# Kernel tuning notes

Measured on AMD Instinct MI355X. Metric: run time of the kernel, lower is better.

## Reference

```python
import jax, jax.numpy as jnp
import numpy as np

B, S, HID = 1, 2048, 2048
H, KVH, D, VD = 32, 8, 128, 128
R = 64  # rope_dim = head_dim * partial_rotary_factor, rounded down to even
N_REP = H // KVH
SCALE = D ** -0.5
NEG = -1e9


def _rotate_half(x):
    half = x.shape[-1] // 2
    return jnp.concatenate([-x[..., half:], x[..., :half]], axis=-1)


def setup_inputs() -> dict:
    key = jax.random.key(0)
    ks = jax.random.split(key, 8)
    hidden_states = jax.random.normal(ks[0], (B, S, HID), dtype=jnp.float32)
    # RoPE angles: standard inverse-frequency positional embedding of width R
    inv_freq = 1.0 / (10000.0 ** (np.arange(0, R, 2, dtype=np.float32) / R))
    pos = np.arange(S, dtype=np.float32)
    freqs = np.outer(pos, inv_freq)                       # [S, R/2]
    emb = np.concatenate([freqs, freqs], axis=-1)         # [S, R]
    cos = jnp.asarray(np.cos(emb))[None].repeat(B, axis=0)  # [B, S, R]
    sin = jnp.asarray(np.sin(emb))[None].repeat(B, axis=0)
    # additive causal mask [B, 1, S, S]
    causal = jnp.triu(jnp.full((S, S), NEG, dtype=jnp.float32), k=1)
    attention_mask = jnp.broadcast_to(causal[None, None], (B, 1, S, S))
    std = 0.02
    Wq = jax.random.normal(ks[1], (H * D, HID), dtype=jnp.float32) * std
    Wk = jax.random.normal(ks[2], (KVH * D, HID), dtype=jnp.float32) * std
    Wv = jax.random.normal(ks[3], (KVH * VD, HID), dtype=jnp.float32) * std
    Wo = jax.random.normal(ks[4], (HID, H * VD), dtype=jnp.float32) * std
    sink_bias = jax.random.normal(ks[5], (H,), dtype=jnp.float32) * 0.5
    return {"hidden_states": hidden_states, "cos": cos, "sin": sin,
            "attention_mask": attention_mask, "Wq": Wq, "Wk": Wk, "Wv": Wv,
            "Wo": Wo, "sink_bias": sink_bias}


def reference(hidden_states, cos, sin, attention_mask, Wq, Wk, Wv, Wo, sink_bias):
    b, s, _ = hidden_states.shape
    # projections -> [B, heads, S, dim]
    q = (hidden_states @ Wq.T).reshape(b, s, H, D).transpose(0, 2, 1, 3)
    k = (hidden_states @ Wk.T).reshape(b, s, KVH, D).transpose(0, 2, 1, 3)
    v = (hidden_states @ Wv.T).reshape(b, s, KVH, VD).transpose(0, 2, 1, 3)
    # partial RoPE on first R dims
    c = cos[:, None, :, :]  # [B,1,S,R]
    si = sin[:, None, :, :]
    q_r, q_n = q[..., :R], q[..., R:]
    k_r, k_n = k[..., :R], k[..., R:]
    q = jnp.concatenate([q_r * c + _rotate_half(q_r) * si, q_n], axis=-1)
    k = jnp.concatenate([k_r * c + _rotate_half(k_r) * si, k_n], axis=-1)
    # GQA: repeat kv heads
    k_rep = jnp.repeat(k, N_REP, axis=1)
    v_rep = jnp.repeat(v, N_REP, axis=1)
    scores = jnp.einsum('bhqd,bhkd->bhqk', q, k_rep) * SCALE + attention_mask
    # extra attention-sink logit column per head
    sinks = jnp.broadcast_to(sink_bias.reshape(1, H, 1, 1), (b, H, s, 1))
    aw = jnp.concatenate([scores, sinks], axis=-1)            # [B,H,S,S+1]
    probs = jax.nn.softmax(aw, axis=-1)[..., :-1]             # drop sink column
    out = jnp.einsum('bhqk,bhkd->bhqd', probs, v_rep)
    out = out.transpose(0, 2, 1, 3).reshape(b, s, H * VD)
    return out @ Wo.T
```

## Files before the change

kernel.cpp:

```cpp
#include <hip/hip_runtime.h>

typedef unsigned short u16;
typedef unsigned int   u32;
typedef __bf16  bf16x8 __attribute__((ext_vector_type(8)));
typedef float   f32x4  __attribute__((ext_vector_type(4)));
typedef float   f32x16 __attribute__((ext_vector_type(16)));
typedef u16     u16x4  __attribute__((ext_vector_type(4)));
typedef u16     u16x8  __attribute__((ext_vector_type(8)));
typedef u32     u32x4  __attribute__((ext_vector_type(4)));

#define S_LEN 2048
#define NH 32
#define NKVH 8
#define HD 128
#define QKVST 6144
#define AOST  4096
#define ATT_SCALE 0.08838834764831845f
#define LOG2E 1.4426950408889634f
#define QSC2 (ATT_SCALE * LOG2E)
#define RESCALE_THR2 11.5f
#define PARTSZ 16640

__device__ __forceinline__ u16 f2bf(float f){
  u32 u = __builtin_bit_cast(u32, f);
  u += 0x7FFFu + ((u >> 16) & 1u);
  return (u16)(u >> 16);
}
__device__ __forceinline__ float bf2f(u16 h){
  u32 u = ((u32)h) << 16;
  return __builtin_bit_cast(float, u);
}
__device__ __forceinline__ u32 cvtpk(float lo, float hi){
  u32 d;
  asm("v_cvt_pk_bf16_f32 %0, %1, %2" : "=v"(d) : "v"(lo), "v"(hi));
  return d;
}
__device__ __forceinline__ void gload_lds16(const u16* g, u16* l){
  __builtin_amdgcn_global_load_lds(
      (const __attribute__((address_space(1))) void*)g,
      (__attribute__((address_space(3))) void*)l, 16, 0, 0);
}

__global__ void cvt_all_kernel(const f32x4* __restrict__ hs, const f32x4* __restrict__ wq,
                               const f32x4* __restrict__ wk, const f32x4* __restrict__ wv,
                               const f32x4* __restrict__ wo, u16x4* __restrict__ out){
  int i = blockIdx.x * 256 + threadIdx.x;
  const f32x4* src; int off;
  if      (i < 1048576){ src = hs; off = i; }
  else if (i < 3145728){ src = wq; off = i - 1048576; }
  else if (i < 3670016){ src = wk; off = i - 3145728; }
  else if (i < 4194304){ src = wv; off = i - 3670016; }
  else                 { src = wo; off = i - 4194304; }
  f32x4 v = src[off];
  u16x4 o;
  o[0] = f2bf(v[0]); o[1] = f2bf(v[1]); o[2] = f2bf(v[2]); o[3] = f2bf(v[3]);
  out[i] = o;
}

template<int OUT_BF16, int ROPE, int BM, int BN, int BK>
__global__ __launch_bounds__(256, 2)
void gemm_bt_kernel(const u16* __restrict__ X, const u16* __restrict__ W,
                    void* __restrict__ Cv, int M, int N, int K,
                    const float* __restrict__ cosv, const float* __restrict__ sinv){
  const int NS = BK / 32;
  __shared__ __align__(16) u16 As[2][NS][BM * 32];
  __shared__ __align__(16) u16 Bs[2][NS][BN * 32];
  const int MI = BM / 32, NJ = BN / 32;
  const int m0 = blockIdx.y * BM, n0 = blockIdx.x * BN;
  const int tid = threadIdx.x;
  const int wave = tid >> 6, lane = tid & 63;
  const int wm = wave >> 1, wn = wave & 1;
  const int g = lane >> 4, ln = lane & 15;
  const int r0 = tid >> 2;
  const int cc = (((tid & 3) ^ ((r0 >> 1) & 3)) * 8);
  f32x4 acc[MI][NJ] = {};
  const u16* xa0 = X + (size_t)(m0 + r0) * K + cc;
  const u16* xa1 = X + (size_t)(m0 + r0 + 64) * K + (((tid & 3) ^ (((r0 + 64) >> 1) & 3)) * 8);
  const u16* wb0 = W + (size_t)(n0 + r0) * K + cc;
  const u16* wb1 = W + (size_t)(n0 + r0 + 64) * K + (((tid & 3) ^ (((r0 + 64) >> 1) & 3)) * 8);

  auto stage = [&](int buf, int k0){
    #pragma unroll
    for (int s = 0; s < NS; s++){
      const int kc = k0 + s * 32;
      gload_lds16(xa0 + kc, &As[buf][s][tid * 8]);
      if (BM == 128) gload_lds16(xa1 + kc, &As[buf][s][2048 + tid * 8]);
      gload_lds16(wb0 + kc, &Bs[buf][s][tid * 8]);
      if (BN == 128) gload_lds16(wb1 + kc, &Bs[buf][s][2048 + tid * 8]);
    }
  };

  stage(0, 0);
  __syncthreads();
  int cur = 0;
  for (int k0 = 0; k0 < K; k0 += BK){
    if (k0 + BK < K) stage(cur ^ 1, k0 + BK);
    #pragma unroll
    for (int s = 0; s < NS; s++){
      bf16x8 a[MI], b[NJ];
      #pragma unroll
      for (int f = 0; f < MI; f++){
        const int row = wm * (BM / 2) + f * 16 + ln;
        a[f] = *(const bf16x8*)&As[cur][s][row * 32 + ((g ^ ((row >> 1) & 3)) * 8)];
      }
      #pragma unroll
      for (int f = 0; f < NJ; f++){
        const int row = wn * (BN / 2) + f * 16 + ln;
        b[f] = *(const bf16x8*)&Bs[cur][s][row * 32 + ((g ^ ((row >> 1) & 3)) * 8)];
      }
      __builtin_amdgcn_s_setprio(1);
      #pragma unroll
      for (int i = 0; i < MI; i++)
        #pragma unroll
        for (int j = 0; j < NJ; j++)
          acc[i][j] = __builtin_amdgcn_mfma_f32_16x16x32_bf16(a[i], b[j], acc[i][j], 0, 0, 0);
      __builtin_amdgcn_s_setprio(0);
    }
    __syncthreads();
    cur ^= 1;
  }
  if (ROPE && BN == 128){
    if (wn == 0 && n0 < 5120){
      #pragma unroll
      for (int i = 0; i < MI; i++)
        #pragma unroll
        for (int r = 0; r < 4; r++){
          const int row = m0 + wm * (BM / 2) + i * 16 + g * 4 + r;
          #pragma unroll
          for (int j = 0; j < 2; j++){
            const int d = j * 16 + ln;
            float c  = cosv[row * 64 + d];
            float sn = sinv[row * 64 + d];
            float x0 = acc[i][j][r], x1 = acc[i][j + 2][r];
            acc[i][j][r]     = x0 * c - x1 * sn;
            acc[i][j + 2][r] = x1 * c + x0 * sn;
          }
        }
    }
    if (n0 < 4096){
      #pragma unroll
      for (int i = 0; i < MI; i++)
        #pragma unroll
        for (int j = 0; j < NJ; j++)
          #pragma unroll
          for (int r = 0; r < 4; r++) acc[i][j][r] *= QSC2;
    }
  }
  #pragma unroll
  for (int i = 0; i < MI; i++)
    #pragma unroll
    for (int j = 0; j < NJ; j++)
      #pragma unroll
      for (int r = 0; r < 4; r++){
        int row = m0 + wm * (BM / 2) + i * 16 + g * 4 + r;
        int col = n0 + wn * (BN / 2) + j * 16 + ln;
        if (OUT_BF16) ((u16*)Cv)[(size_t)row * N + col] = f2bf(acc[i][j][r]);
        else          ((float*)Cv)[(size_t)row * N + col] = acc[i][j][r];
      }
}

__global__ void vtrans_kernel(const u16* __restrict__ QKV, u16* __restrict__ VT){
  int idx = blockIdx.x * 256 + threadIdx.x;
  if (idx >= NKVH * HD * S_LEN) return;
  int s   = idx & (S_LEN - 1);
  int vd  = (idx >> 11) & (HD - 1);
  int kvh = idx >> 18;
  VT[idx] = QKV[(size_t)s * QKVST + 5120 + kvh * HD + vd];
}

__global__ __launch_bounds__(256, 2)
void attn_kernel(const u16* __restrict__ QKV, const u16* __restrict__ VT,
                 const float* __restrict__ sinkb, u16* __restrict__ AO,
                 u16* __restrict__ PART){
  __shared__ __align__(16) u16 Ks[2][32 * 256];
  __shared__ __align__(16) u16 Vs[2][32 * 256];
  const int b    = blockIdx.x;
  const int kvh  = b & 7;
  const int head = kvh * 4 + ((b >> 3) & 3);
  const int p    = (b >> 5) & 7;
  const int role = b >> 8;
  const int qtL  = 15 - p;
  const int tid  = threadIdx.x;
  const int w    = tid >> 6;
  const int lane = tid & 63;
  const int l31  = lane & 31, hi = lane >> 5;

  const u16* Kbase = QKV + 4096 + kvh * HD;
  const u16* Vbase = VT + (size_t)kvh * HD * S_LEN;

  auto stage = [&](int buf, int kt){
    const int k0 = kt * 64;
    #pragma unroll
    for (int pp = 0; pp < 4; pp++){
      int idx = pp * 256 + tid;
      int r = idx >> 5, c = idx & 31;
      int cs = c ^ r;
      int key = r * 2 + (cs >> 4), d8 = (cs & 15) * 8;
      gload_lds16(Kbase + (size_t)(k0 + key) * QKVST + d8, &Ks[buf][idx * 8]);
    }
    #pragma unroll
    for (int pp = 0; pp < 4; pp++){
      int idx = pp * 256 + tid;
      int r = idx >> 5, c = idx & 31;
      int cs = c ^ r;
      int vd = r * 4 + (cs >> 3), k8 = (cs & 7) * 8;
      gload_lds16(Vbase + (size_t)vd * S_LEN + k0 + k8, &Vs[buf][idx * 8]);
    }
  };

  const float sb2 = sinkb[head] * LOG2E;
  bf16x8 qB[8];
  float m, Ll;
  f32x16 O[4];

  auto load_q = [&](int q0){
    const int qw = q0 + w * 32;
    const u16* qrow = QKV + (size_t)(qw + l31) * QKVST + head * HD;
    #pragma unroll
    for (int t = 0; t < 8; t++) qB[t] = *(const bf16x8*)(qrow + t * 16 + hi * 8);
    #pragma unroll
    for (int n = 0; n < 4; n++) O[n] = f32x16{};
  };

  auto do_tile = [&](int cur, int k0, int qw){
    const u16* Kc = Ks[cur];
    const u16* Vc = Vs[cur];
    f32x16 sc0 = {}, sc1 = {};
    const int krow0 = (l31 >> 1);
    const int kc0   = ((l31 & 1) << 4) | hi;
    __builtin_amdgcn_s_setprio(1);
    #pragma unroll
    for (int t = 0; t < 8; t++){
      bf16x8 ka0 = *(const bf16x8*)&Kc[krow0 * 256 + ((kc0 + 2 * t) ^ krow0) * 8];
      bf16x8 ka1 = *(const bf16x8*)&Kc[(16 + krow0) * 256 + ((kc0 + 2 * t) ^ (16 + krow0)) * 8];
      sc0 = __builtin_amdgcn_mfma_f32_32x32x16_bf16(ka0, qB[t], sc0, 0, 0, 0);
      sc1 = __builtin_amdgcn_mfma_f32_32x32x16_bf16(ka1, qB[t], sc1, 0, 0, 0);
    }
    __builtin_amdgcn_s_setprio(0);

    if (k0 + 63 > qw){
      const int qg = qw + l31;
      #pragma unroll
      for (int r = 0; r < 16; r++){
        int keyr = k0 + (r & 3) + 8 * (r >> 2) + 4 * hi;
        if (keyr      > qg) sc0[r] = -1e30f;
        if (keyr + 32 > qg) sc1[r] = -1e30f;
      }
    }
    float mx = sc0[0];
    #pragma unroll
    for (int r = 1; r < 16; r++) mx = fmaxf(mx, sc0[r]);
    #pragma unroll
    for (int r = 0; r < 16; r++) mx = fmaxf(mx, sc1[r]);
    mx = fmaxf(mx, __shfl_xor(mx, 32));
    if (!__all(mx <= m + RESCALE_THR2)){
      float mn = fmaxf(m, mx);
      float sf = exp2f(m - mn);
      m = mn;
      #pragma unroll
      for (int n = 0; n < 4; n++)
        #pragma unroll
        for (int r = 0; r < 16; r++) O[n][r] *= sf;
      Ll *= sf;
    }
    float p0[16], p1[16];
    #pragma unroll
    for (int r = 0; r < 16; r++){ p0[r] = exp2f(sc0[r] - m); Ll += p0[r]; }
    #pragma unroll
    for (int r = 0; r < 16; r++){ p1[r] = exp2f(sc1[r] - m); Ll += p1[r]; }

    __builtin_amdgcn_s_setprio(1);
    #pragma unroll
    for (int c = 0; c < 4; c++){
      const float* ps = (c & 2) ? p1 : p0;
      const int bb = (c & 1) * 8;
      u32 wa = cvtpk(ps[bb + 0], ps[bb + 1]);
      u32 wb = cvtpk(ps[bb + 2], ps[bb + 3]);
      u32 wc = cvtpk(ps[bb + 4], ps[bb + 5]);
      u32 wd = cvtpk(ps[bb + 6], ps[bb + 7]);
      asm("v_permlane32_swap_b32 %0, %1" : "+v"(wa), "+v"(wc));
      asm("v_permlane32_swap_b32 %0, %1" : "+v"(wb), "+v"(wd));
      u32x4 wv_; wv_[0] = wa; wv_[1] = wb; wv_[2] = wc; wv_[3] = wd;
      bf16x8 pf = __builtin_bit_cast(bf16x8, wv_);
      #pragma unroll
      for (int n = 0; n < 4; n++){
        const int vrow = n * 8 + (l31 >> 2);
        const int vcc  = ((l31 & 3) << 3) | (c << 1) | hi;
        bf16x8 va = *(const bf16x8*)&Vc[vrow * 256 + (vcc ^ vrow) * 8];
        O[n] = __builtin_amdgcn_mfma_f32_32x32x16_bf16(va, pf, O[n], 0, 0, 0);
      }
    }
    __builtin_amdgcn_s_setprio(0);
  };

  auto run = [&](int q0, int kt0, int kt1){
    const int qw = q0 + w * 32;
    stage(0, kt0);
    __syncthreads();
    int cur = 0;
    for (int kt = kt0; kt < kt1; kt++){
      if (kt + 1 < kt1) stage(cur ^ 1, kt + 1);
      if (kt * 64 < qw + 32) do_tile(cur, kt * 64, qw);
      __syncthreads();
      cur ^= 1;
    }
  };

  auto epilogue = [&](int q0, bool final_, int rr_){
    float l = Ll + __shfl_xor(Ll, 32);
    float inv, lse;
    if (l > 0.f){ inv = 1.f / l; lse = m + __log2f(l); }
    else        { inv = 0.f;     lse = -1e30f; }
    u16* arena = &Ks[0][0];
    #pragma unroll
    for (int n = 0; n < 4; n++)
      #pragma unroll
      for (int r = 0; r < 16; r++){
        int vd = n * 32 + (r & 3) + 8 * (r >> 2) + 4 * hi;
        int ch = (vd >> 3) ^ (l31 & 15);
        arena[w * 4096 + l31 * 128 + ch * 8 + (vd & 7)] = f2bf(O[n][r] * inv);
      }
    __syncthreads();
    if (final_){
      #pragma unroll
      for (int pp = 0; pp < 8; pp++){
        int idx = pp * 256 + tid;
        int row = idx >> 4, c = idx & 15;
        u16x8 v = *(const u16x8*)&arena[row * 128 + ((c ^ (row & 15)) * 8)];
        *(u16x8*)&AO[(size_t)(q0 + row) * AOST + head * HD + c * 8] = v;
      }
    } else {
      u16* base = PART + (size_t)((head * 8 + p) * 2 + rr_) * PARTSZ;
      #pragma unroll
      for (int pp = 0; pp < 8; pp++){
        int idx = pp * 256 + tid;
        int row = idx >> 4, c = idx & 15;
        u16x8 v = *(const u16x8*)&arena[row * 128 + ((c ^ (row & 15)) * 8)];
        *(u16x8*)&base[row * 128 + c * 8] = v;
      }
      if (hi == 0) ((float*)(base + 16384))[w * 32 + l31] = lse;
    }
    __syncthreads();
  };

  const int q0L = qtL * 128;
  if (role == 0){
    load_q(q0L);
    m = sb2; Ll = (hi == 0) ? 1.f : 0.f;
    run(q0L, 0, 18);
    epilogue(q0L, false, 0);
  } else {
    load_q(q0L);
    m = -3.0e38f; Ll = 0.f;
    run(q0L, 18, 32 - 2 * p);
    epilogue(q0L, false, 1);
    const int q0S = p * 128;
    load_q(q0S);
    m = sb2; Ll = (hi == 0) ? 1.f : 0.f;
    run(q0S, 0, 2 * p + 2);
    epilogue(q0S, true, 0);
  }
}

__global__ void merge_kernel(const u16* __restrict__ PART, u16* __restrict__ AO){
  const int sidx = blockIdx.x;
  const int h = sidx >> 3, p = sidx & 7;
  const int q0 = (15 - p) * 128;
  const u16* A = PART + (size_t)(sidx * 2 + 0) * PARTSZ;
  const u16* B = PART + (size_t)(sidx * 2 + 1) * PARTSZ;
  const float* lseA = (const float*)(A + 16384);
  const float* lseB = (const float*)(B + 16384);
  #pragma unroll
  for (int it = 0; it < 8; it++){
    int idx = it * 256 + threadIdx.x;
    int row = idx >> 4, c = (idx & 15) * 8;
    float la = lseA[row], lb = lseB[row];
    float mx = fmaxf(la, lb);
    float wa = exp2f(la - mx), wb = exp2f(lb - mx);
    float inv = 1.f / (wa + wb);
    u16x8 va = *(const u16x8*)&A[row * 128 + c];
    u16x8 vb = *(const u16x8*)&B[row * 128 + c];
    u16x8 o;
    #pragma unroll
    for (int j = 0; j < 8; j++)
      o[j] = f2bf((bf2f(va[j]) * wa + bf2f(vb[j]) * wb) * inv);
    *(u16x8*)&AO[(size_t)(q0 + row) * AOST + h * HD + c] = o;
  }
}

extern "C" void kernel_launch(void* const* d_in, const int* in_sizes, int n_in,
                              void* d_out, int out_size, void* d_ws, size_t ws_size,
                              hipStream_t stream){
  (void)in_sizes; (void)n_in; (void)out_size; (void)ws_size;
  const float* hs    = (const float*)d_in[0];
  const float* cosv  = (const float*)d_in[1];
  const float* sinv  = (const float*)d_in[2];
  const float* Wq    = (const float*)d_in[4];
  const float* Wk    = (const float*)d_in[5];
  const float* Wv    = (const float*)d_in[6];
  const float* Wo    = (const float*)d_in[7];
  const float* sinkb = (const float*)d_in[8];
  float* out = (float*)d_out;

  char* ws = (char*)d_ws;
  u16* XB    = (u16*)(ws);
  u16* WQKVB = (u16*)(ws + 8388608);
  u16* WOB   = (u16*)(ws + 33554432);
  u16* QKV   = (u16*)(ws + 50331648);
  u16* VT    = (u16*)(ws + 75497472);
  u16* AO    = (u16*)(ws + 79691776);
  u16* PART  = (u16*)(ws);

  cvt_all_kernel<<<24576, 256, 0, stream>>>((const f32x4*)hs, (const f32x4*)Wq,
                                            (const f32x4*)Wk, (const f32x4*)Wv,
                                            (const f32x4*)Wo, (u16x4*)ws);

  gemm_bt_kernel<1, 1, 128, 128, 32><<<dim3(48, 16), 256, 0, stream>>>(XB, WQKVB, QKV, 2048, 6144, 2048, cosv, sinv);

  vtrans_kernel<<<8192, 256, 0, stream>>>(QKV, VT);

  attn_kernel<<<dim3(512), 256, 0, stream>>>(QKV, VT, sinkb, AO, PART);

  merge_kernel<<<dim3(256), 256, 0, stream>>>(PART, AO);

  gemm_bt_kernel<0, 0, 128, 64, 64><<<dim3(32, 16), 256, 0, stream>>>(AO, WOB, out, 2048, 2048, 4096, nullptr, nullptr);
}
```

Before: 220.0 us.

## Share K/V tiles across the four GQA heads in one 512-thread attention block

The attention kernel now runs 512-thread blocks in which 8 waves cover all four query heads of a KV group (2 waves per head, 64 query rows). Each K/V tile is staged into LDS once and used by all four heads, where before a separate block per head loaded it. The causal split into long/short query tiles and the partial-result merge are reworked for 64-row tiles, giving half as many blocks and larger partial buffers. The aim is to cut redundant K/V global loads, at the cost of fewer, larger blocks and possibly lower occupancy and load balance on the GPU.

```diff
diff --git a/kernel.cpp b/kernel.cpp
--- a/kernel.cpp
+++ b/kernel.cpp
@@ -19,7 +19,7 @@
 #define LOG2E 1.4426950408889634f
 #define QSC2 (ATT_SCALE * LOG2E)
 #define RESCALE_THR2 11.5f
-#define PARTSZ 16640
+#define PARTSZ 33280
 
 __device__ __forceinline__ u16 f2bf(float f){
   u32 u = __builtin_bit_cast(u32, f);
@@ -168,20 +168,19 @@
   VT[idx] = QKV[(size_t)s * QKVST + 5120 + kvh * HD + vd];
 }
 
-__global__ __launch_bounds__(256, 2)
+__global__ __launch_bounds__(512, 2)
 void attn_kernel(const u16* __restrict__ QKV, const u16* __restrict__ VT,
                  const float* __restrict__ sinkb, u16* __restrict__ AO,
                  u16* __restrict__ PART){
-  __shared__ __align__(16) u16 Ks[2][32 * 256];
-  __shared__ __align__(16) u16 Vs[2][32 * 256];
+  __shared__ __align__(16) u16 lds[4][32 * 256];
   const int b    = blockIdx.x;
   const int kvh  = b & 7;
-  const int head = kvh * 4 + ((b >> 3) & 3);
-  const int p    = (b >> 5) & 7;
-  const int role = b >> 8;
-  const int qtL  = 15 - p;
+  const int s    = (b >> 3) & 15;
+  const int role = b >> 7;
+  const int qtL  = 31 - s;
   const int tid  = threadIdx.x;
   const int w    = tid >> 6;
+  const int head = kvh * 4 + (w >> 1);
   const int lane = tid & 63;
   const int l31  = lane & 31, hi = lane >> 5;
 
@@ -191,20 +190,20 @@
   auto stage = [&](int buf, int kt){
     const int k0 = kt * 64;
     #pragma unroll
-    for (int pp = 0; pp < 4; pp++){
-      int idx = pp * 256 + tid;
+    for (int pp = 0; pp < 2; pp++){
+      int idx = pp * 512 + tid;
       int r = idx >> 5, c = idx & 31;
       int cs = c ^ r;
       int key = r * 2 + (cs >> 4), d8 = (cs & 15) * 8;
-      gload_lds16(Kbase + (size_t)(k0 + key) * QKVST + d8, &Ks[buf][idx * 8]);
-    }
-    #pragma unroll
-    for (int pp = 0; pp < 4; pp++){
-      int idx = pp * 256 + tid;
+      gload_lds16(Kbase + (size_t)(k0 + key) * QKVST + d8, &lds[buf][idx * 8]);
+    }
+    #pragma unroll
+    for (int pp = 0; pp < 2; pp++){
+      int idx = pp * 512 + tid;
       int r = idx >> 5, c = idx & 31;
       int cs = c ^ r;
       int vd = r * 4 + (cs >> 3), k8 = (cs & 7) * 8;
-      gload_lds16(Vbase + (size_t)vd * S_LEN + k0 + k8, &Vs[buf][idx * 8]);
+      gload_lds16(Vbase + (size_t)vd * S_LEN + k0 + k8, &lds[2 + buf][idx * 8]);
     }
   };
 
@@ -214,7 +213,7 @@
   f32x16 O[4];
 
   auto load_q = [&](int q0){
-    const int qw = q0 + w * 32;
+    const int qw = q0 + (w & 1) * 32;
     const u16* qrow = QKV + (size_t)(qw + l31) * QKVST + head * HD;
     #pragma unroll
     for (int t = 0; t < 8; t++) qB[t] = *(const bf16x8*)(qrow + t * 16 + hi * 8);
@@ -223,8 +222,8 @@
   };
 
   auto do_tile = [&](int cur, int k0, int qw){
-    const u16* Kc = Ks[cur];
-    const u16* Vc = Vs[cur];
+    const u16* Kc = lds[cur];
+    const u16* Vc = lds[2 + cur];
     f32x16 sc0 = {}, sc1 = {};
     const int krow0 = (l31 >> 1);
     const int kc0   = ((l31 & 1) << 4) | hi;
@@ -294,7 +293,8 @@
   };
 
   auto run = [&](int q0, int kt0, int kt1){
-    const int qw = q0 + w * 32;
+    if (kt0 >= kt1) return;
+    const int qw = q0 + (w & 1) * 32;
     stage(0, kt0);
     __syncthreads();
     int cur = 0;
@@ -306,72 +306,73 @@
     }
   };
 
-  auto epilogue = [&](int q0, bool final_, int rr_){
+  auto epilogue = [&](int q0, bool final_, int rec){
     float l = Ll + __shfl_xor(Ll, 32);
     float inv, lse;
     if (l > 0.f){ inv = 1.f / l; lse = m + __log2f(l); }
     else        { inv = 0.f;     lse = -1e30f; }
-    u16* arena = &Ks[0][0];
+    u16* arena = &lds[0][0];
+    const int rr = w * 32 + l31;
     #pragma unroll
     for (int n = 0; n < 4; n++)
       #pragma unroll
       for (int r = 0; r < 16; r++){
         int vd = n * 32 + (r & 3) + 8 * (r >> 2) + 4 * hi;
         int ch = (vd >> 3) ^ (l31 & 15);
-        arena[w * 4096 + l31 * 128 + ch * 8 + (vd & 7)] = f2bf(O[n][r] * inv);
+        arena[rr * 128 + ch * 8 + (vd & 7)] = f2bf(O[n][r] * inv);
       }
     __syncthreads();
     if (final_){
       #pragma unroll
       for (int pp = 0; pp < 8; pp++){
-        int idx = pp * 256 + tid;
+        int idx = pp * 512 + tid;
         int row = idx >> 4, c = idx & 15;
         u16x8 v = *(const u16x8*)&arena[row * 128 + ((c ^ (row & 15)) * 8)];
-        *(u16x8*)&AO[(size_t)(q0 + row) * AOST + head * HD + c * 8] = v;
+        *(u16x8*)&AO[(size_t)(q0 + (row & 63)) * AOST + (kvh * 4 + (row >> 6)) * HD + c * 8] = v;
       }
     } else {
-      u16* base = PART + (size_t)((head * 8 + p) * 2 + rr_) * PARTSZ;
+      u16* base = PART + (size_t)((kvh * 16 + s) * 2 + rec) * PARTSZ;
       #pragma unroll
       for (int pp = 0; pp < 8; pp++){
-        int idx = pp * 256 + tid;
+        int idx = pp * 512 + tid;
         int row = idx >> 4, c = idx & 15;
         u16x8 v = *(const u16x8*)&arena[row * 128 + ((c ^ (row & 15)) * 8)];
         *(u16x8*)&base[row * 128 + c * 8] = v;
       }
-      if (hi == 0) ((float*)(base + 16384))[w * 32 + l31] = lse;
+      if (hi == 0) ((float*)(base + 32768))[rr] = lse;
     }
     __syncthreads();
   };
 
-  const int q0L = qtL * 128;
+  const int q0L = qtL * 64;
   if (role == 0){
     load_q(q0L);
     m = sb2; Ll = (hi == 0) ? 1.f : 0.f;
-    run(q0L, 0, 18);
+    run(q0L, 0, 17);
     epilogue(q0L, false, 0);
   } else {
     load_q(q0L);
     m = -3.0e38f; Ll = 0.f;
-    run(q0L, 18, 32 - 2 * p);
+    run(q0L, 17, 32 - s);
     epilogue(q0L, false, 1);
-    const int q0S = p * 128;
+    const int q0S = s * 64;
     load_q(q0S);
     m = sb2; Ll = (hi == 0) ? 1.f : 0.f;
-    run(q0S, 0, 2 * p + 2);
+    run(q0S, 0, s + 1);
     epilogue(q0S, true, 0);
   }
 }
 
 __global__ void merge_kernel(const u16* __restrict__ PART, u16* __restrict__ AO){
   const int sidx = blockIdx.x;
-  const int h = sidx >> 3, p = sidx & 7;
-  const int q0 = (15 - p) * 128;
+  const int kvh = sidx >> 4, s = sidx & 15;
+  const int q0 = (31 - s) * 64;
   const u16* A = PART + (size_t)(sidx * 2 + 0) * PARTSZ;
   const u16* B = PART + (size_t)(sidx * 2 + 1) * PARTSZ;
-  const float* lseA = (const float*)(A + 16384);
-  const float* lseB = (const float*)(B + 16384);
+  const float* lseA = (const float*)(A + 32768);
+  const float* lseB = (const float*)(B + 32768);
   #pragma unroll
-  for (int it = 0; it < 8; it++){
+  for (int it = 0; it < 16; it++){
     int idx = it * 256 + threadIdx.x;
     int row = idx >> 4, c = (idx & 15) * 8;
     float la = lseA[row], lb = lseB[row];
@@ -384,7 +385,7 @@
     #pragma unroll
     for (int j = 0; j < 8; j++)
       o[j] = f2bf((bf2f(va[j]) * wa + bf2f(vb[j]) * wb) * inv);
-    *(u16x8*)&AO[(size_t)(q0 + row) * AOST + h * HD + c] = o;
+    *(u16x8*)&AO[(size_t)(q0 + (row & 63)) * AOST + (kvh * 4 + (row >> 6)) * HD + c] = o;
   }
 }
 
@@ -419,9 +420,9 @@
 
   vtrans_kernel<<<8192, 256, 0, stream>>>(QKV, VT);
 
-  attn_kernel<<<dim3(512), 256, 0, stream>>>(QKV, VT, sinkb, AO, PART);
-
-  merge_kernel<<<dim3(256), 256, 0, stream>>>(PART, AO);
+  attn_kernel<<<dim3(256), 512, 0, stream>>>(QKV, VT, sinkb, AO, PART);
+
+  merge_kernel<<<dim3(128), 256, 0, stream>>>(PART, AO);
 
   gemm_bt_kernel<0, 0, 128, 64, 64><<<dim3(32, 16), 256, 0, stream>>>(AO, WOB, out, 2048, 2048, 4096, nullptr, nullptr);
 }
```

Measured after the change: 214.6 us. -2.4%, faster.
